# Performance work log

Hardware: AMD Instinct MI355X
Metric: run time of the kernel (lower is better)

The kernel has to match this reference:

```python
import jax, jax.numpy as jnp
import numpy as np

EMBED = 768
HEADS = 12
HID = EMBED * HEADS  # 9216; head_dim == embed_dim in this module
EPS = 1e-5


def _layernorm(x, g, b):
    mu = jnp.mean(x, axis=-1, keepdims=True)
    var = jnp.mean(jnp.square(x - mu), axis=-1, keepdims=True)
    return (x - mu) * jax.lax.rsqrt(var + EPS) * g + b


def setup_inputs() -> dict:
    key = jax.random.key(0)
    ks = jax.random.split(key, 16)
    B, S = 4, 1024
    s_in = 1.0 / np.sqrt(EMBED)
    s_hid = 1.0 / np.sqrt(HID)
    return {
        "x": jax.random.normal(ks[0], (B, S, EMBED), jnp.float32),
        "ln1_g": jnp.ones((EMBED,), jnp.float32),
        "ln1_b": jnp.zeros((EMBED,), jnp.float32),
        "wq": jax.random.normal(ks[1], (EMBED, HID), jnp.float32) * s_in,
        "bq": jnp.zeros((HID,), jnp.float32),
        "wk": jax.random.normal(ks[2], (EMBED, HID), jnp.float32) * s_in,
        "bk": jnp.zeros((HID,), jnp.float32),
        "wv": jax.random.normal(ks[3], (EMBED, HID), jnp.float32) * s_in,
        "bv": jnp.zeros((HID,), jnp.float32),
        "wo": jax.random.normal(ks[4], (HID, EMBED), jnp.float32) * s_hid,
        "bo": jnp.zeros((EMBED,), jnp.float32),
        "ln2_g": jnp.ones((EMBED,), jnp.float32),
        "ln2_b": jnp.zeros((EMBED,), jnp.float32),
        "w1": jax.random.normal(ks[5], (EMBED, EMBED), jnp.float32) * s_in,
        "b1": jnp.zeros((EMBED,), jnp.float32),
        "w2": jax.random.normal(ks[6], (EMBED, EMBED), jnp.float32) * s_in,
        "b2": jnp.zeros((EMBED,), jnp.float32),
    }


def reference(x, ln1_g, ln1_b, wq, bq, wk, bk, wv, bv, wo, bo,
              ln2_g, ln2_b, w1, b1, w2, b2):
    B, S, D = x.shape
    H = HEADS
    nx = _layernorm(x, ln1_g, ln1_b)
    # QKV projections: each head gets a FULL embed_dim-wide slice (head_dim == D)
    q = (nx @ wq + bq).reshape(B, S, H, D)
    k = (nx @ wk + bk).reshape(B, S, H, D)
    v = (nx @ wv + bv).reshape(B, S, H, D)
    scores = jnp.einsum("bqhd,bkhd->bhqk", q, k) / jnp.sqrt(jnp.float32(D))
    # Original applies softmax over dim=1 of per-head [B,q,k] scores -> the QUERY axis
    attn = jax.nn.softmax(scores, axis=-2)
    ctx = jnp.einsum("bhqk,bkhd->bqhd", attn, v).reshape(B, S, H * D)
    x_att = ctx @ wo + bo
    x = x + x_att
    h = _layernorm(x, ln2_g, ln2_b)
    h = jax.nn.gelu(h @ w1 + b1, approximate=False)
    h = h @ w2 + b2
    return x + h
```

## Files before the change

kernel.cpp:

```cpp
#include <hip/hip_runtime.h>
#include <math.h>

#define D_EMB 768
#define HEADS 12
#define HID   9216
#define BATCH 4
#define SEQ   1024
#define M_ROWS 4096

typedef __attribute__((ext_vector_type(8))) short bf16x8;
typedef __attribute__((ext_vector_type(4))) float f32x4;

__device__ __forceinline__ float b2f(unsigned short u) {
    return __uint_as_float(((unsigned)u) << 16);
}
__device__ __forceinline__ unsigned short f2b(float f) {
    unsigned u = __float_as_uint(f);
    u += 0x7fffu + ((u >> 16) & 1u);
    return (unsigned short)(u >> 16);
}

__device__ __forceinline__ void async_copy16(const void* g, void* l) {
    __builtin_amdgcn_global_load_lds(
        (const __attribute__((address_space(1))) void*)g,
        (__attribute__((address_space(3))) void*)l, 16, 0, 0);
}

enum { EPI_BF16 = 0, EPI_SCALE_BF16 = 1, EPI_BIAS_BF16 = 2,
       EPI_BIAS_GELU_BF16 = 3, EPI_BIAS_RES_F32 = 4, EPI_F32_PART = 5,
       EPI_QKV = 6 };

template<int EPI, int SWAP = 0>
__global__ __launch_bounds__(256)
void gemm_bt(const unsigned short* __restrict__ A,
             const unsigned short* __restrict__ B,
             void* __restrict__ Cv,
             void* __restrict__ p2,
             void* __restrict__ p3,
             const float* __restrict__ bias,
             const float* __restrict__ bias2,
             const float* __restrict__ bias3,
             const float* __restrict__ resid,
             float scale, int K, int ksplit,
             int lda, int ldb, int ldc, int nh,
             long sAb, long sAh, long sBb, long sBh, long sCb, long sCh)
{
    __shared__ unsigned short As[2][128 * 32];
    __shared__ unsigned short Bs[2][128 * 32];

    const int bz = blockIdx.z;
    int Kloop = K;
    const unsigned short* Ab;
    const unsigned short* Bb;
    long coff;
    if constexpr (EPI == EPI_F32_PART) {
        Ab = A + (long)bz * ksplit;
        Bb = B + (long)bz * ksplit;
        coff = (long)bz * sCb;
        Kloop = ksplit;
    } else {
        const int b = bz / nh, h = bz - b * nh;
        Ab = A + (long)b * sAb + (long)h * sAh;
        Bb = B + (long)b * sBb + (long)h * sBh;
        coff = (long)b * sCb + (long)h * sCh;
    }

    const int bm = SWAP ? blockIdx.x : blockIdx.y;
    const int bn = SWAP ? blockIdx.y : blockIdx.x;
    const int tid = threadIdx.x;
    const int c0 = tid, c1 = tid + 256;

    const unsigned short* Ap0 = Ab + (long)(bm * 128 + (c0 >> 2)) * lda + (c0 & 3) * 8;
    const unsigned short* Ap1 = Ab + (long)(bm * 128 + (c1 >> 2)) * lda + (c1 & 3) * 8;
    const unsigned short* Bp0 = Bb + (long)(bn * 128 + (c0 >> 2)) * ldb + (c0 & 3) * 8;
    const unsigned short* Bp1 = Bb + (long)(bn * 128 + (c1 >> 2)) * ldb + (c1 & 3) * 8;

    const int lane = tid & 63;
    const int wid = tid >> 6;
    const int wm = wid >> 1, wn = wid & 1;
    const int r = lane & 15, ks = lane >> 4;

    f32x4 acc[4][4] = {};

    async_copy16(Ap0, &As[0][c0 * 8]);
    async_copy16(Ap1, &As[0][c1 * 8]);
    async_copy16(Bp0, &Bs[0][c0 * 8]);
    async_copy16(Bp1, &Bs[0][c1 * 8]);
    Ap0 += 32; Ap1 += 32; Bp0 += 32; Bp1 += 32;
    __syncthreads();

    int cur = 0;
    for (int kt = 0; kt < Kloop; kt += 32) {
        if (kt + 32 < Kloop) {
            const int nxt = cur ^ 1;
            async_copy16(Ap0, &As[nxt][c0 * 8]);
            async_copy16(Ap1, &As[nxt][c1 * 8]);
            async_copy16(Bp0, &Bs[nxt][c0 * 8]);
            async_copy16(Bp1, &Bs[nxt][c1 * 8]);
            Ap0 += 32; Ap1 += 32; Bp0 += 32; Bp1 += 32;
        }

        bf16x8 af[4], bfr[4];
        #pragma unroll
        for (int m = 0; m < 4; m++)
            af[m] = *(const bf16x8*)&As[cur][(wm * 64 + m * 16 + r) * 32 + ks * 8];
        #pragma unroll
        for (int n = 0; n < 4; n++)
            bfr[n] = *(const bf16x8*)&Bs[cur][(wn * 64 + n * 16 + r) * 32 + ks * 8];

        #pragma unroll
        for (int m = 0; m < 4; m++)
            #pragma unroll
            for (int n = 0; n < 4; n++)
                acc[m][n] = __builtin_amdgcn_mfma_f32_16x16x32_bf16(
                    af[m], bfr[n], acc[m][n], 0, 0, 0);

        __syncthreads();
        cur ^= 1;
    }

    int third = 0;
    if constexpr (EPI == EPI_QKV) third = (bn * 128) / ldc;

    #pragma unroll
    for (int m = 0; m < 4; m++) {
        const int row0 = bm * 128 + wm * 64 + m * 16 + ks * 4;
        #pragma unroll
        for (int n = 0; n < 4; n++) {
            const int col = bn * 128 + wn * 64 + n * 16 + r;
            #pragma unroll
            for (int j = 0; j < 4; j++) {
                const int row = row0 + j;
                float v = acc[m][n][j];
                if constexpr (EPI == EPI_SCALE_BF16) v *= scale;
                if constexpr (EPI == EPI_BIAS_BF16 || EPI == EPI_BIAS_GELU_BF16 ||
                              EPI == EPI_BIAS_RES_F32) v += bias[col];
                if constexpr (EPI == EPI_BIAS_GELU_BF16)
                    v = 0.5f * v * (1.0f + erff(v * 0.70710678118654752f));
                if constexpr (EPI == EPI_BIAS_RES_F32) {
                    float* C = (float*)Cv;
                    C[coff + (long)row * ldc + col] = v + resid[(long)row * ldc + col];
                } else if constexpr (EPI == EPI_F32_PART) {
                    float* C = (float*)Cv;
                    C[coff + (long)row * ldc + col] = v;
                } else if constexpr (EPI == EPI_QKV) {
                    const int cl = col - third * ldc;
                    unsigned short* C = (third == 0) ? (unsigned short*)Cv
                                      : (third == 1) ? (unsigned short*)p2
                                                     : (unsigned short*)p3;
                    const float* bs = (third == 0) ? bias : (third == 1) ? bias2 : bias3;
                    C[(long)row * ldc + cl] = f2b(v + bs[cl]);
                } else {
                    unsigned short* C = (unsigned short*)Cv;
                    C[coff + (long)row * ldc + col] = f2b(v);
                }
            }
        }
    }
}

__global__ __launch_bounds__(256)
void reduce_part(const f32x4* __restrict__ p, f32x4* __restrict__ x2,
                 int n4, int nsp)
{
    const int i = blockIdx.x * 256 + threadIdx.x;
    f32x4 a = x2[i];
    for (int s = 0; s < nsp; s++) {
        const f32x4 v = p[(long)s * n4 + i];
        a[0] += v[0]; a[1] += v[1]; a[2] += v[2]; a[3] += v[3];
    }
    x2[i] = a;
}

__global__ __launch_bounds__(256)
void transpose_w(const float* __restrict__ in, unsigned short* __restrict__ out,
                 int R, int C, int col0)
{
    __shared__ float t[32][33];
    const int c0 = blockIdx.x * 32, r0 = blockIdx.y * 32;
    const int tx = threadIdx.x & 31, ty = threadIdx.x >> 5;
    #pragma unroll
    for (int i = 0; i < 4; i++)
        t[ty + i * 8][tx] = in[(long)(r0 + ty + i * 8) * C + col0 + c0 + tx];
    __syncthreads();
    #pragma unroll
    for (int i = 0; i < 4; i++)
        out[(long)(c0 + ty + i * 8) * R + r0 + tx] = f2b(t[tx][ty + i * 8]);
}

__global__ __launch_bounds__(256)
void transpose_v(const unsigned short* __restrict__ v, unsigned short* __restrict__ vt,
                 int ng)
{
    __shared__ unsigned short t[32][34];
    const int bz = blockIdx.z;
    const int b = bz / ng, hl = bz - b * ng;
    const int d0 = blockIdx.x * 32, s0 = blockIdx.y * 32;
    const int tx = threadIdx.x & 31, ty = threadIdx.x >> 5;
    const int ld = ng * D_EMB;
    const unsigned short* vin = v + (long)b * SEQ * ld + (long)hl * D_EMB;
    #pragma unroll
    for (int i = 0; i < 4; i++)
        t[ty + i * 8][tx] = vin[(long)(s0 + ty + i * 8) * ld + d0 + tx];
    __syncthreads();
    unsigned short* vo = vt + (long)bz * D_EMB * SEQ;
    #pragma unroll
    for (int i = 0; i < 4; i++)
        vo[(long)(d0 + ty + i * 8) * SEQ + s0 + tx] = t[tx][ty + i * 8];
}

__global__ __launch_bounds__(256)
void ln_kernel(const float* __restrict__ x, const float* __restrict__ g,
               const float* __restrict__ bb, unsigned short* __restrict__ out)
{
    const int row = blockIdx.x;
    const float* xr = x + (long)row * D_EMB;
    const int t = threadIdx.x;
    float v0 = xr[t], v1 = xr[t + 256], v2 = xr[t + 512];
    float s = v0 + v1 + v2;
    float ss = v0 * v0 + v1 * v1 + v2 * v2;
    #pragma unroll
    for (int o = 32; o > 0; o >>= 1) {
        s += __shfl_down(s, o);
        ss += __shfl_down(ss, o);
    }
    __shared__ float red[8];
    __shared__ float mu_s, rs_s;
    const int wid = t >> 6;
    if ((t & 63) == 0) { red[wid] = s; red[4 + wid] = ss; }
    __syncthreads();
    if (t == 0) {
        float a = red[0] + red[1] + red[2] + red[3];
        float q = red[4] + red[5] + red[6] + red[7];
        float mu = a * (1.0f / D_EMB);
        float var = q * (1.0f / D_EMB) - mu * mu;
        mu_s = mu;
        rs_s = rsqrtf(var + 1e-5f);
    }
    __syncthreads();
    const float mu = mu_s, rs = rs_s;
    unsigned short* orow = out + (long)row * D_EMB;
    orow[t]       = f2b((v0 - mu) * rs * g[t]       + bb[t]);
    orow[t + 256] = f2b((v1 - mu) * rs * g[t + 256] + bb[t + 256]);
    orow[t + 512] = f2b((v2 - mu) * rs * g[t + 512] + bb[t + 512]);
}

__global__ __launch_bounds__(256)
void x2_init(const float* __restrict__ x, const float* __restrict__ bo,
             float* __restrict__ x2)
{
    const int row = blockIdx.x;
    const float* xr = x + (long)row * D_EMB;
    float* o = x2 + (long)row * D_EMB;
    const int t = threadIdx.x;
    o[t]       = xr[t]       + bo[t];
    o[t + 256] = xr[t + 256] + bo[t + 256];
    o[t + 512] = xr[t + 512] + bo[t + 512];
}

__global__ __launch_bounds__(256)
void col_softmax(unsigned short* __restrict__ s)
{
    const long base = (long)blockIdx.y * ((long)SEQ * SEQ);
    const int t63 = threadIdx.x & 63;
    const int part = threadIdx.x >> 6;
    const int col = blockIdx.x * 64 + t63;
    unsigned short* p = s + base + col;
    const int q0 = part * 256;
    float m = -1e30f, sum = 0.0f;
    for (int q = q0; q < q0 + 256; q++) {
        float v = b2f(p[(long)q * SEQ]);
        float mn = fmaxf(m, v);
        sum = sum * __expf(m - mn) + __expf(v - mn);
        m = mn;
    }
    __shared__ float lm[4][64], ls[4][64];
    lm[part][t63] = m;
    ls[part][t63] = sum;
    __syncthreads();
    const float M = fmaxf(fmaxf(lm[0][t63], lm[1][t63]),
                          fmaxf(lm[2][t63], lm[3][t63]));
    const float S = ls[0][t63] * __expf(lm[0][t63] - M)
                  + ls[1][t63] * __expf(lm[1][t63] - M)
                  + ls[2][t63] * __expf(lm[2][t63] - M)
                  + ls[3][t63] * __expf(lm[3][t63] - M);
    const float inv = 1.0f / S;
    for (int q = q0; q < q0 + 256; q++) {
        float v = b2f(p[(long)q * SEQ]);
        p[(long)q * SEQ] = f2b(__expf(v - M) * inv);
    }
}

extern "C" void kernel_launch(void* const* d_in, const int* in_sizes, int n_in,
                              void* d_out, int out_size, void* d_ws, size_t ws_size,
                              hipStream_t stream)
{
    const float* x    = (const float*)d_in[0];
    const float* ln1g = (const float*)d_in[1];
    const float* ln1b = (const float*)d_in[2];
    const float* wq   = (const float*)d_in[3];
    const float* bq   = (const float*)d_in[4];
    const float* wk   = (const float*)d_in[5];
    const float* bk   = (const float*)d_in[6];
    const float* wv   = (const float*)d_in[7];
    const float* bv   = (const float*)d_in[8];
    const float* wo   = (const float*)d_in[9];
    const float* bo   = (const float*)d_in[10];
    const float* ln2g = (const float*)d_in[11];
    const float* ln2b = (const float*)d_in[12];
    const float* w1   = (const float*)d_in[13];
    const float* b1   = (const float*)d_in[14];
    const float* w2   = (const float*)d_in[15];
    const float* b2   = (const float*)d_in[16];
    float* out = (float*)d_out;

    auto a256 = [](size_t b) { return (b + 255) & ~(size_t)255; };

    auto plan_bytes = [&](int g) -> size_t {
        size_t o = 0;
        o += a256((size_t)D_EMB * D_EMB * 2);
        o += a256((size_t)D_EMB * D_EMB * 2);
        o += a256((size_t)M_ROWS * D_EMB * 2);
        o += a256((size_t)M_ROWS * D_EMB * 2);
        o += a256((size_t)M_ROWS * D_EMB * 4);
        o += a256((size_t)3 * g * D_EMB * D_EMB * 2);
        o += 4 * a256((size_t)M_ROWS * (size_t)g * D_EMB * 2);
        o += a256((size_t)BATCH * g * SEQ * SEQ * 2);
        return o;
    };
    const int cand[6] = {12, 6, 4, 3, 2, 1};
    int G = 1;
    for (int i = 0; i < 6; i++) {
        if (plan_bytes(cand[i]) <= ws_size) { G = cand[i]; break; }
    }
    const int NG = G * D_EMB;

    char* ws = (char*)d_ws;
    size_t off = 0;
    auto alloc = [&](size_t bytes) {
        void* p = ws + off;
        off += a256(bytes);
        return p;
    };
    unsigned short* w1T = (unsigned short*)alloc((size_t)D_EMB * D_EMB * 2);
    unsigned short* w2T = (unsigned short*)alloc((size_t)D_EMB * D_EMB * 2);
    unsigned short* nx  = (unsigned short*)alloc((size_t)M_ROWS * D_EMB * 2);
    unsigned short* h1  = (unsigned short*)alloc((size_t)M_ROWS * D_EMB * 2);
    float* x2           = (float*)alloc((size_t)M_ROWS * D_EMB * 4);
    unsigned short* wsl = (unsigned short*)alloc((size_t)3 * NG * D_EMB * 2);
    unsigned short* qg  = (unsigned short*)alloc((size_t)M_ROWS * NG * 2);
    unsigned short* kg  = (unsigned short*)alloc((size_t)M_ROWS * NG * 2);
    unsigned short* vtg = (unsigned short*)alloc((size_t)M_ROWS * NG * 2);
    unsigned short* ctg = (unsigned short*)alloc((size_t)M_ROWS * NG * 2);
    unsigned short* scg = (unsigned short*)alloc((size_t)BATCH * G * SEQ * SEQ * 2);

    const size_t part_one = (size_t)M_ROWS * D_EMB * 4;
    const size_t avail = 3 * (size_t)M_ROWS * NG * 2;
    int nsp = 4;
    while (nsp > 1 && (size_t)nsp * part_one > avail) nsp >>= 1;
    while (nsp > 1 && (NG / nsp) % 32 != 0) nsp >>= 1;
    float* part = (float*)qg;

    const dim3 blk(256);
    const float scl = 0.03608439182435161f;

    ln_kernel<<<dim3(M_ROWS), blk, 0, stream>>>(x, ln1g, ln1b, nx);
    x2_init<<<dim3(M_ROWS), blk, 0, stream>>>(x, bo, x2);
    transpose_w<<<dim3(D_EMB / 32, D_EMB / 32), blk, 0, stream>>>(w1, w1T, D_EMB, D_EMB, 0);
    transpose_w<<<dim3(D_EMB / 32, D_EMB / 32), blk, 0, stream>>>(w2, w2T, D_EMB, D_EMB, 0);

    const int ngrp = HEADS / G;
    for (int g = 0; g < ngrp; g++) {
        const int h0 = g * G;
        transpose_w<<<dim3(NG / 32, D_EMB / 32), blk, 0, stream>>>(wq, wsl, D_EMB, HID, h0 * D_EMB);
        transpose_w<<<dim3(NG / 32, D_EMB / 32), blk, 0, stream>>>(wk, wsl + (size_t)NG * D_EMB, D_EMB, HID, h0 * D_EMB);
        transpose_w<<<dim3(NG / 32, D_EMB / 32), blk, 0, stream>>>(wv, wsl + (size_t)2 * NG * D_EMB, D_EMB, HID, h0 * D_EMB);

        gemm_bt<EPI_QKV, 1><<<dim3(M_ROWS / 128, 3 * NG / 128, 1), blk, 0, stream>>>(
            nx, wsl, qg, kg, ctg,
            bq + h0 * D_EMB, bk + h0 * D_EMB, bv + h0 * D_EMB, nullptr,
            1.0f, D_EMB, 0, D_EMB, D_EMB, NG, 1, 0, 0, 0, 0, 0, 0);
        transpose_v<<<dim3(D_EMB / 32, SEQ / 32, BATCH * G), blk, 0, stream>>>(ctg, vtg, G);

        gemm_bt<EPI_SCALE_BF16><<<dim3(SEQ / 128, SEQ / 128, BATCH * G), blk, 0, stream>>>(
            qg, kg, scg, nullptr, nullptr, nullptr, nullptr, nullptr, nullptr,
            scl, D_EMB, 0, NG, NG, SEQ, G,
            (long)SEQ * NG, D_EMB, (long)SEQ * NG, D_EMB,
            (long)G * SEQ * SEQ, (long)SEQ * SEQ);

        col_softmax<<<dim3(SEQ / 64, BATCH * G), blk, 0, stream>>>(scg);

        gemm_bt<EPI_BF16><<<dim3(D_EMB / 128, SEQ / 128, BATCH * G), blk, 0, stream>>>(
            scg, vtg, ctg, nullptr, nullptr, nullptr, nullptr, nullptr, nullptr,
            1.0f, SEQ, 0, SEQ, SEQ, NG, G,
            (long)G * SEQ * SEQ, (long)SEQ * SEQ,
            (long)G * D_EMB * SEQ, (long)D_EMB * SEQ,
            (long)SEQ * NG, (long)D_EMB);

        transpose_w<<<dim3(D_EMB / 32, NG / 32), blk, 0, stream>>>(
            wo + (long)h0 * D_EMB * D_EMB, wsl, NG, D_EMB, 0);
        gemm_bt<EPI_F32_PART><<<dim3(D_EMB / 128, M_ROWS / 128, nsp), blk, 0, stream>>>(
            ctg, wsl, part, nullptr, nullptr, nullptr, nullptr, nullptr, nullptr,
            1.0f, NG, NG / nsp, NG, NG, D_EMB, 1,
            0, 0, 0, 0, (long)M_ROWS * D_EMB, 0);
        reduce_part<<<dim3(M_ROWS * D_EMB / 4 / 256), blk, 0, stream>>>(
            (const f32x4*)part, (f32x4*)x2, M_ROWS * D_EMB / 4, nsp);
    }

    ln_kernel<<<dim3(M_ROWS), blk, 0, stream>>>(x2, ln2g, ln2b, nx);

    gemm_bt<EPI_BIAS_GELU_BF16><<<dim3(D_EMB / 128, M_ROWS / 128, 1), blk, 0, stream>>>(
        nx, w1T, h1, nullptr, nullptr, b1, nullptr, nullptr, nullptr,
        1.0f, D_EMB, 0, D_EMB, D_EMB, D_EMB, 1, 0, 0, 0, 0, 0, 0);

    gemm_bt<EPI_BIAS_RES_F32><<<dim3(D_EMB / 128, M_ROWS / 128, 1), blk, 0, stream>>>(
        h1, w2T, out, nullptr, nullptr, b2, nullptr, nullptr, x2,
        1.0f, D_EMB, 0, D_EMB, D_EMB, D_EMB, 1, 0, 0, 0, 0, 0, 0);
}
```

Measured before the change: 927.4 us.

## Split fused QKV GEMM and alias V-raw with score buffer to shrink workspace

Replaces the single fused QKV GEMM, which picked the destination and bias per column third, with three separate bias GEMMs. The raw V buffer now shares memory with the score buffer, and ctx reuses the Q buffer. The smaller per-group workspace may let a larger head group G fit, which means fewer loop iterations and kernel launches. It adds two extra launches per group, and the larger buffer needs for the partial-sum split may lower nsp.

Measured after the change: 915.6 us. No clear change (-1.3%).

```diff
diff --git a/kernel.cpp b/kernel.cpp
--- a/kernel.cpp
+++ b/kernel.cpp
@@ -27,19 +27,14 @@
 }
 
 enum { EPI_BF16 = 0, EPI_SCALE_BF16 = 1, EPI_BIAS_BF16 = 2,
-       EPI_BIAS_GELU_BF16 = 3, EPI_BIAS_RES_F32 = 4, EPI_F32_PART = 5,
-       EPI_QKV = 6 };
+       EPI_BIAS_GELU_BF16 = 3, EPI_BIAS_RES_F32 = 4, EPI_F32_PART = 5 };
 
 template<int EPI, int SWAP = 0>
 __global__ __launch_bounds__(256)
 void gemm_bt(const unsigned short* __restrict__ A,
              const unsigned short* __restrict__ B,
              void* __restrict__ Cv,
-             void* __restrict__ p2,
-             void* __restrict__ p3,
              const float* __restrict__ bias,
-             const float* __restrict__ bias2,
-             const float* __restrict__ bias3,
              const float* __restrict__ resid,
              float scale, int K, int ksplit,
              int lda, int ldb, int ldc, int nh,
@@ -118,9 +113,6 @@
         __syncthreads();
         cur ^= 1;
     }
-
-    int third = 0;
-    if constexpr (EPI == EPI_QKV) third = (bn * 128) / ldc;
 
     #pragma unroll
     for (int m = 0; m < 4; m++) {
@@ -143,13 +135,6 @@
                 } else if constexpr (EPI == EPI_F32_PART) {
                     float* C = (float*)Cv;
                     C[coff + (long)row * ldc + col] = v;
-                } else if constexpr (EPI == EPI_QKV) {
-                    const int cl = col - third * ldc;
-                    unsigned short* C = (third == 0) ? (unsigned short*)Cv
-                                      : (third == 1) ? (unsigned short*)p2
-                                                     : (unsigned short*)p3;
-                    const float* bs = (third == 0) ? bias : (third == 1) ? bias2 : bias3;
-                    C[(long)row * ldc + cl] = f2b(v + bs[cl]);
                 } else {
                     unsigned short* C = (unsigned short*)Cv;
                     C[coff + (long)row * ldc + col] = f2b(v);
@@ -324,8 +309,10 @@
         o += a256((size_t)M_ROWS * D_EMB * 2);
         o += a256((size_t)M_ROWS * D_EMB * 4);
         o += a256((size_t)3 * g * D_EMB * D_EMB * 2);
-        o += 4 * a256((size_t)M_ROWS * (size_t)g * D_EMB * 2);
-        o += a256((size_t)BATCH * g * SEQ * SEQ * 2);
+        o += 3 * a256((size_t)M_ROWS * (size_t)g * D_EMB * 2);
+        size_t vr = (size_t)M_ROWS * (size_t)g * D_EMB * 2;
+        size_t sc = (size_t)BATCH * g * SEQ * SEQ * 2;
+        o += a256(vr > sc ? vr : sc);
         return o;
     };
     const int cand[6] = {12, 6, 4, 3, 2, 1};
@@ -351,15 +338,21 @@
     unsigned short* qg  = (unsigned short*)alloc((size_t)M_ROWS * NG * 2);
     unsigned short* kg  = (unsigned short*)alloc((size_t)M_ROWS * NG * 2);
     unsigned short* vtg = (unsigned short*)alloc((size_t)M_ROWS * NG * 2);
-    unsigned short* ctg = (unsigned short*)alloc((size_t)M_ROWS * NG * 2);
-    unsigned short* scg = (unsigned short*)alloc((size_t)BATCH * G * SEQ * SEQ * 2);
+    {
+        size_t vr = (size_t)M_ROWS * NG * 2;
+        size_t sc = (size_t)BATCH * G * SEQ * SEQ * 2;
+        (void)alloc(vr > sc ? vr : sc);
+    }
+    unsigned short* vr  = vtg + (size_t)M_ROWS * NG;
+    unsigned short* scg = vr;
+    unsigned short* ctx = qg;
 
     const size_t part_one = (size_t)M_ROWS * D_EMB * 4;
-    const size_t avail = 3 * (size_t)M_ROWS * NG * 2;
+    const size_t avail = 2 * (size_t)M_ROWS * NG * 2;
     int nsp = 4;
     while (nsp > 1 && (size_t)nsp * part_one > avail) nsp >>= 1;
     while (nsp > 1 && (NG / nsp) % 32 != 0) nsp >>= 1;
-    float* part = (float*)qg;
+    float* part = (float*)kg;
 
     const dim3 blk(256);
     const float scl = 0.03608439182435161f;
@@ -372,18 +365,26 @@
     const int ngrp = HEADS / G;
     for (int g = 0; g < ngrp; g++) {
         const int h0 = g * G;
-        transpose_w<<<dim3(NG / 32, D_EMB / 32), blk, 0, stream>>>(wq, wsl, D_EMB, HID, h0 * D_EMB);
-        transpose_w<<<dim3(NG / 32, D_EMB / 32), blk, 0, stream>>>(wk, wsl + (size_t)NG * D_EMB, D_EMB, HID, h0 * D_EMB);
-        transpose_w<<<dim3(NG / 32, D_EMB / 32), blk, 0, stream>>>(wv, wsl + (size_t)2 * NG * D_EMB, D_EMB, HID, h0 * D_EMB);
-
-        gemm_bt<EPI_QKV, 1><<<dim3(M_ROWS / 128, 3 * NG / 128, 1), blk, 0, stream>>>(
-            nx, wsl, qg, kg, ctg,
-            bq + h0 * D_EMB, bk + h0 * D_EMB, bv + h0 * D_EMB, nullptr,
+        unsigned short* wslQ = wsl;
+        unsigned short* wslK = wsl + (size_t)NG * D_EMB;
+        unsigned short* wslV = wsl + (size_t)2 * NG * D_EMB;
+        transpose_w<<<dim3(NG / 32, D_EMB / 32), blk, 0, stream>>>(wq, wslQ, D_EMB, HID, h0 * D_EMB);
+        transpose_w<<<dim3(NG / 32, D_EMB / 32), blk, 0, stream>>>(wk, wslK, D_EMB, HID, h0 * D_EMB);
+        transpose_w<<<dim3(NG / 32, D_EMB / 32), blk, 0, stream>>>(wv, wslV, D_EMB, HID, h0 * D_EMB);
+
+        gemm_bt<EPI_BIAS_BF16, 1><<<dim3(M_ROWS / 128, NG / 128, 1), blk, 0, stream>>>(
+            nx, wslQ, qg, bq + h0 * D_EMB, nullptr,
             1.0f, D_EMB, 0, D_EMB, D_EMB, NG, 1, 0, 0, 0, 0, 0, 0);
-        transpose_v<<<dim3(D_EMB / 32, SEQ / 32, BATCH * G), blk, 0, stream>>>(ctg, vtg, G);
+        gemm_bt<EPI_BIAS_BF16, 1><<<dim3(M_ROWS / 128, NG / 128, 1), blk, 0, stream>>>(
+            nx, wslK, kg, bk + h0 * D_EMB, nullptr,
+            1.0f, D_EMB, 0, D_EMB, D_EMB, NG, 1, 0, 0, 0, 0, 0, 0);
+        gemm_bt<EPI_BIAS_BF16, 1><<<dim3(M_ROWS / 128, NG / 128, 1), blk, 0, stream>>>(
+            nx, wslV, vr, bv + h0 * D_EMB, nullptr,
+            1.0f, D_EMB, 0, D_EMB, D_EMB, NG, 1, 0, 0, 0, 0, 0, 0);
+        transpose_v<<<dim3(D_EMB / 32, SEQ / 32, BATCH * G), blk, 0, stream>>>(vr, vtg, G);
 
         gemm_bt<EPI_SCALE_BF16><<<dim3(SEQ / 128, SEQ / 128, BATCH * G), blk, 0, stream>>>(
-            qg, kg, scg, nullptr, nullptr, nullptr, nullptr, nullptr, nullptr,
+            qg, kg, scg, nullptr, nullptr,
             scl, D_EMB, 0, NG, NG, SEQ, G,
             (long)SEQ * NG, D_EMB, (long)SEQ * NG, D_EMB,
             (long)G * SEQ * SEQ, (long)SEQ * SEQ);
@@ -391,7 +392,7 @@
         col_softmax<<<dim3(SEQ / 64, BATCH * G), blk, 0, stream>>>(scg);
 
         gemm_bt<EPI_BF16><<<dim3(D_EMB / 128, SEQ / 128, BATCH * G), blk, 0, stream>>>(
-            scg, vtg, ctg, nullptr, nullptr, nullptr, nullptr, nullptr, nullptr,
+            scg, vtg, ctx, nullptr, nullptr,
             1.0f, SEQ, 0, SEQ, SEQ, NG, G,
             (long)G * SEQ * SEQ, (long)SEQ * SEQ,
             (long)G * D_EMB * SEQ, (long)D_EMB * SEQ,
@@ -400,7 +401,7 @@
         transpose_w<<<dim3(D_EMB / 32, NG / 32), blk, 0, stream>>>(
             wo + (long)h0 * D_EMB * D_EMB, wsl, NG, D_EMB, 0);
         gemm_bt<EPI_F32_PART><<<dim3(D_EMB / 128, M_ROWS / 128, nsp), blk, 0, stream>>>(
-            ctg, wsl, part, nullptr, nullptr, nullptr, nullptr, nullptr, nullptr,
+            ctx, wsl, part, nullptr, nullptr,
             1.0f, NG, NG / nsp, NG, NG, D_EMB, 1,
             0, 0, 0, 0, (long)M_ROWS * D_EMB, 0);
         reduce_part<<<dim3(M_ROWS * D_EMB / 4 / 256), blk, 0, stream>>>(
@@ -410,10 +411,10 @@
     ln_kernel<<<dim3(M_ROWS), blk, 0, stream>>>(x2, ln2g, ln2b, nx);
 
     gemm_bt<EPI_BIAS_GELU_BF16><<<dim3(D_EMB / 128, M_ROWS / 128, 1), blk, 0, stream>>>(
-        nx, w1T, h1, nullptr, nullptr, b1, nullptr, nullptr, nullptr,
+        nx, w1T, h1, b1, nullptr,
         1.0f, D_EMB, 0, D_EMB, D_EMB, D_EMB, 1, 0, 0, 0, 0, 0, 0);
 
     gemm_bt<EPI_BIAS_RES_F32><<<dim3(D_EMB / 128, M_ROWS / 128, 1), blk, 0, stream>>>(
-        h1, w2T, out, nullptr, nullptr, b2, nullptr, nullptr, x2,
+        h1, w2T, out, b2, x2,
         1.0f, D_EMB, 0, D_EMB, D_EMB, D_EMB, 1, 0, 0, 0, 0, 0, 0);
 }
```
